# Kernel tuning notes

Measured on AMD Instinct MI355X. Metric: run time of the kernel, lower is better.

Reference implementation:

```python
import jax, jax.numpy as jnp
import numpy as np

B, T, D, H, K = 8, 1024, 512, 8, 33
DK = D // H
PAD = (K - 1) // 2
EPS = 1e-5


def _ln(x, g, b):
    m = x.mean(-1, keepdims=True)
    v = ((x - m) ** 2).mean(-1, keepdims=True)
    return (x - m) / jnp.sqrt(v + EPS) * g + b


def _ffn(x, g, b, w1, b1, w2, b2):
    h = jax.nn.silu(_ln(x, g, b) @ w1 + b1)
    return h @ w2 + b2


def _rel_shift(x):
    # x: [B, H, T1, T2]
    b, h, t1, t2 = x.shape
    x = jnp.pad(x, ((0, 0), (0, 0), (0, 0), (1, 0)))
    x = x.reshape(b, h, t2 + 1, t1)[:, :, 1:, :].reshape(b, h, t1, t2)
    return x[..., :t1]


def setup_inputs() -> dict:
    key = jax.random.key(0)
    ks = iter(jax.random.split(key, 40))
    rn = lambda *s: jax.random.normal(next(ks), s, jnp.float32) * 0.02
    inp = {
        'x': jax.random.normal(next(ks), (B, T, D), jnp.float32),
        'pos_emb': jax.random.normal(next(ks), (1, T, D), jnp.float32),
        # ffn1
        'ln1_g': jnp.ones((D,), jnp.float32), 'ln1_b': jnp.zeros((D,), jnp.float32),
        'ffn1_w1': rn(D, 4 * D), 'ffn1_b1': jnp.zeros((4 * D,), jnp.float32),
        'ffn1_w2': rn(4 * D, D), 'ffn1_b2': jnp.zeros((D,), jnp.float32),
        # mhsa
        'lnq_g': jnp.ones((D,), jnp.float32), 'lnq_b': jnp.zeros((D,), jnp.float32),
        'lnk_g': jnp.ones((D,), jnp.float32), 'lnk_b': jnp.zeros((D,), jnp.float32),
        'lnv_g': jnp.ones((D,), jnp.float32), 'lnv_b': jnp.zeros((D,), jnp.float32),
        'wq': rn(D, D), 'wk': rn(D, D), 'wv': rn(D, D), 'wpos': rn(D, D),
        'pos_bias_u': jnp.zeros((H, DK), jnp.float32),
        'pos_bias_v': jnp.zeros((H, DK), jnp.float32),
        'wfc': rn(D, D),
        # conv module
        'cln_g': jnp.ones((D,), jnp.float32), 'cln_b': jnp.zeros((D,), jnp.float32),
        'pw1': rn(D, 4 * D),             # pointwise_conv1 weight as [in, out]
        'dw_w': rn(2 * D, 1, K),         # depthwise conv weight [C, 1, K]
        'bn_g': jnp.ones((2 * D,), jnp.float32), 'bn_b': jnp.zeros((2 * D,), jnp.float32),
        'pw2': rn(2 * D, D),
        # ffn2
        'ln2_g': jnp.ones((D,), jnp.float32), 'ln2_b': jnp.zeros((D,), jnp.float32),
        'ffn2_w1': rn(D, 4 * D), 'ffn2_b1': jnp.zeros((4 * D,), jnp.float32),
        'ffn2_w2': rn(4 * D, D), 'ffn2_b2': jnp.zeros((D,), jnp.float32),
        # final layer norm
        'lnf_g': jnp.ones((D,), jnp.float32), 'lnf_b': jnp.zeros((D,), jnp.float32),
    }
    return inp


def reference(x, pos_emb, ln1_g, ln1_b, ffn1_w1, ffn1_b1, ffn1_w2, ffn1_b2,
              lnq_g, lnq_b, lnk_g, lnk_b, lnv_g, lnv_b, wq, wk, wv, wpos,
              pos_bias_u, pos_bias_v, wfc,
              cln_g, cln_b, pw1, dw_w, bn_g, bn_b, pw2,
              ln2_g, ln2_b, ffn2_w1, ffn2_b1, ffn2_w2, ffn2_b2, lnf_g, lnf_b):
    b, t, d = x.shape
    scale = 1.0 / DK ** 0.5

    # ---- FFN1 (half-step) ----
    out = 0.5 * x + 0.5 * (x + _ffn(x, ln1_g, ln1_b, ffn1_w1, ffn1_b1, ffn1_w2, ffn1_b2))

    # ---- rel-pos MHSA ----
    res = out
    q = (_ln(out, lnq_g, lnq_b) @ wq).reshape(b, t, H, DK)            # [B,T,H,dk]
    k = (_ln(out, lnk_g, lnk_b) @ wk).reshape(b, t, H, DK).transpose(0, 2, 1, 3)
    v = (_ln(out, lnv_g, lnv_b) @ wv).reshape(b, t, H, DK).transpose(0, 2, 1, 3)
    p = (pos_emb @ wpos).reshape(pos_emb.shape[0], -1, H, DK).transpose(0, 2, 3, 1)  # [1,H,dk,Tp]

    q_u = (q + pos_bias_u).transpose(0, 2, 1, 3)                      # [B,H,T,dk]
    q_v = (q + pos_bias_v).transpose(0, 2, 1, 3)
    matrix_bd = _rel_shift(jnp.matmul(q_v, p) * scale)                # [B,H,T,T]
    scores = jnp.einsum('bhqd,bhkd->bhqk', q_u, k) * scale + matrix_bd
    attn = jax.nn.softmax(scores, axis=-1)
    o = jnp.einsum('bhqk,bhkd->bhqd', attn, v)
    out = o.transpose(0, 2, 1, 3).reshape(b, t, d) @ wfc + res

    # ---- convolution module ----
    res = out
    h = _ln(out, cln_g, cln_b) @ pw1                                  # [B,T,4D]
    a, g = jnp.split(h, 2, axis=-1)
    h = a * jax.nn.sigmoid(g)                                         # GLU -> [B,T,2D]
    h = jax.lax.conv_general_dilated(
        h.transpose(0, 2, 1), dw_w, window_strides=(1,),
        padding=[(PAD, PAD)], feature_group_count=2 * D,
        dimension_numbers=('NCH', 'OIH', 'NCH')).transpose(0, 2, 1)
    h = jax.nn.silu(_ln(h, bn_g, bn_b))
    out = h @ pw2 + res

    # ---- FFN2 (half-step) + final LN ----
    out = 0.5 * out + 0.5 * (out + _ffn(out, ln2_g, ln2_b, ffn2_w1, ffn2_b1, ffn2_w2, ffn2_b2))
    return _ln(out, lnf_g, lnf_b)
```

## Files before the change

kernel.cpp:

```cpp
#include <hip/hip_runtime.h>

typedef unsigned short bf16u;
typedef __attribute__((ext_vector_type(8))) short bf16x8;
typedef __attribute__((ext_vector_type(4))) float f32x4;

__device__ __forceinline__ float bf2f(bf16u u) {
    return __uint_as_float(((unsigned)u) << 16);
}
__device__ __forceinline__ bf16u f2bf(float f) {
    unsigned u = __float_as_uint(f);
    unsigned r = (u + 0x7fffu + ((u >> 16) & 1u)) >> 16;
    return (bf16u)r;
}
__device__ __forceinline__ float sigmoidf_(float x) {
    return 1.0f / (1.0f + __expf(-x));
}

__device__ __forceinline__ void gload_lds16(const bf16u* g, bf16u* l) {
    __builtin_amdgcn_global_load_lds(
        (const __attribute__((address_space(1))) unsigned int*)(const void*)g,
        (__attribute__((address_space(3))) unsigned int*)(void*)l, 16, 0, 0);
}

__global__ void init_flag_kernel(int* flag) {
    if (threadIdx.x == 0 && blockIdx.x == 0) *flag = 0;
}
__global__ __launch_bounds__(256) void detect_kernel(
    const void* x, int nelem, int* flag)
{
    const int scan = nelem < (1 << 20) ? nelem : (1 << 20);
    const bf16u* p = (const bf16u*)x;
    int bad = 0;
    for (int j = blockIdx.x * 256 + threadIdx.x; j < scan; j += 65536) {
        unsigned u = p[j];
        if ((u & 0x7F80u) == 0x7F80u) bad = 1;
    }
    if (bad) atomicOr(flag, 1);
}

__global__ __launch_bounds__(256) void cvt_bf_kernel(
    const void* __restrict__ in, bf16u* __restrict__ out, int n,
    const int* __restrict__ flagp)
{
    const int f32 = *flagp;
    const int i = blockIdx.x * 256 + threadIdx.x;
    if (i >= n) return;
    if (f32) out[i] = f2bf(((const float*)in)[i]);
    else     out[i] = ((const bf16u*)in)[i];
}

struct WTab {
    const void* w[11];
    bf16u* wt[11];
    int K[11];
    int N[11];
};
__global__ __launch_bounds__(256) void wtrans_all(
    WTab tab, const int* __restrict__ flagp)
{
    __shared__ float tile[32][33];
    const int id = blockIdx.z;
    const int K = tab.K[id], N = tab.N[id];
    const int n0 = blockIdx.x * 32, k0 = blockIdx.y * 32;
    if (n0 >= N || k0 >= K) return;
    const void* W = tab.w[id];
    bf16u* Wt = tab.wt[id];
    const int f32 = *flagp;
    const int tx = threadIdx.x & 31, ty = threadIdx.x >> 5;
    #pragma unroll
    for (int r = 0; r < 4; ++r) {
        const int k = ty + r * 8;
        float v;
        if (f32) v = ((const float*)W)[(size_t)(k0 + k) * N + n0 + tx];
        else     v = bf2f(((const bf16u*)W)[(size_t)(k0 + k) * N + n0 + tx]);
        tile[k][tx] = v;
    }
    __syncthreads();
    #pragma unroll
    for (int r = 0; r < 4; ++r) {
        const int n = ty + r * 8;
        Wt[(size_t)(n0 + n) * K + k0 + tx] = f2bf(tile[tx][n]);
    }
}

__global__ __launch_bounds__(256) void vtrans_kernel(
    const bf16u* __restrict__ vb, bf16u* __restrict__ vt)
{
    __shared__ bf16u tile[32][33];
    const int j0 = blockIdx.x * 32;
    const int h = blockIdx.y >> 1, dt = (blockIdx.y & 1) * 32;
    const int b = blockIdx.z;
    const int tx = threadIdx.x & 31, ty = threadIdx.x >> 5;
    #pragma unroll
    for (int r = 0; r < 4; ++r) {
        const int j = ty + r * 8;
        tile[j][tx] = vb[(size_t)(b * 1024 + j0 + j) * 512 + h * 64 + dt + tx];
    }
    __syncthreads();
    #pragma unroll
    for (int r = 0; r < 4; ++r) {
        const int d = ty + r * 8;
        vt[(size_t)((b * 8 + h) * 64 + dt + d) * 1024 + j0 + tx] = tile[tx][d];
    }
}

__global__ __launch_bounds__(256) void add_qbias_kernel(
    const bf16u* __restrict__ qb, const void* __restrict__ bu,
    const void* __restrict__ bv, bf16u* __restrict__ qu,
    bf16u* __restrict__ qv, const int* __restrict__ flagp)
{
    const int f32 = *flagp;
    const int idx = blockIdx.x * 256 + threadIdx.x;
    const int c = idx & 511;
    const float q = bf2f(qb[idx]);
    float ub, vbias;
    if (f32) { ub = ((const float*)bu)[c]; vbias = ((const float*)bv)[c]; }
    else     { ub = bf2f(((const bf16u*)bu)[c]); vbias = bf2f(((const bf16u*)bv)[c]); }
    qu[idx] = f2bf(q + ub);
    qv[idx] = f2bf(q + vbias);
}

template <int D, int IN_MODE, int OUT_MODE, bool SILU, bool COPY>
__global__ __launch_bounds__(256) void ln_kernel(
    const void* __restrict__ in_, const void* __restrict__ gvec,
    const void* __restrict__ bvec, void* __restrict__ out_,
    float* __restrict__ copy_out, const int* __restrict__ flagp)
{
    constexpr int VPT = D / 256;
    const int f32 = *flagp;
    const int row = blockIdx.x;
    const int tid = threadIdx.x;
    const size_t base = (size_t)row * D;
    float x[VPT];
    if (IN_MODE == 2 || (IN_MODE == 1 && !f32)) {
        const bf16u* in = (const bf16u*)in_;
        #pragma unroll
        for (int i = 0; i < VPT; ++i) x[i] = bf2f(in[base + tid + i * 256]);
    } else {
        const float* in = (const float*)in_;
        #pragma unroll
        for (int i = 0; i < VPT; ++i) x[i] = in[base + tid + i * 256];
    }
    float s = 0.f, q = 0.f;
    #pragma unroll
    for (int i = 0; i < VPT; ++i) { s += x[i]; q += x[i] * x[i]; }
    __shared__ float red[10];
    #pragma unroll
    for (int off = 32; off; off >>= 1) {
        s += __shfl_down(s, off, 64);
        q += __shfl_down(q, off, 64);
    }
    const int lane = tid & 63, wv = tid >> 6;
    if (lane == 0) { red[wv] = s; red[4 + wv] = q; }
    __syncthreads();
    if (tid == 0) {
        float ts = red[0] + red[1] + red[2] + red[3];
        float tq = red[4] + red[5] + red[6] + red[7];
        float mean = ts / (float)D;
        float var = tq / (float)D - mean * mean;
        red[8] = mean;
        red[9] = rsqrtf(var + 1e-5f);
    }
    __syncthreads();
    const float mean = red[8], rstd = red[9];
    #pragma unroll
    for (int i = 0; i < VPT; ++i) {
        const int c = tid + i * 256;
        float gv, bv;
        if (f32) {
            gv = ((const float*)gvec)[c];
            bv = ((const float*)bvec)[c];
        } else {
            gv = bf2f(((const bf16u*)gvec)[c]);
            bv = bf2f(((const bf16u*)bvec)[c]);
        }
        float v = (x[i] - mean) * rstd * gv + bv;
        if (SILU) v *= sigmoidf_(v);
        if (OUT_MODE == 0) {
            ((bf16u*)out_)[base + c] = f2bf(v);
        } else {
            if (f32) ((float*)out_)[base + c] = v;
            else     ((bf16u*)out_)[base + c] = f2bf(v);
        }
        if (COPY) copy_out[base + c] = x[i];
    }
}

template <int TM>
__global__ __launch_bounds__(256) void gemm_mfma(
    const bf16u* __restrict__ A, const bf16u* __restrict__ Wt,
    const void* __restrict__ bias, const float* __restrict__ res,
    void* __restrict__ C, int M, int N, int K, float alpha, int act,
    int outbf, const int* __restrict__ flagp)
{
    constexpr int CHUNKS_A = TM * 4;
    constexpr int TOT = CHUNKS_A + 512;
    constexpr int CPW = TOT / 4;
    constexpr int ISSUES = CPW / 64;
    constexpr int BUFSZ = (TM + 128) * 32;
    constexpr int MI = 4;
    constexpr int NJ = (TM == 128) ? 4 : 2;
    __shared__ bf16u sh[3 * BUFSZ];
    const int f32 = *flagp;
    const int tid = threadIdx.x;
    const int mtiles = M / TM;
    const int lid = blockIdx.y * gridDim.x + blockIdx.x;
    const int bm = (lid % mtiles) * TM;
    const int bn = (lid / mtiles) * 128;
    const int lane = tid & 63, wvid = tid >> 6;
    const int wm = (TM == 128) ? (wvid >> 1) * 64 : 0;
    const int wn = (TM == 128) ? (wvid & 1) * 64 : wvid * 32;

    f32x4 acc[MI][NJ];
    {
        f32x4 z = {0.f, 0.f, 0.f, 0.f};
        #pragma unroll
        for (int i = 0; i < MI; ++i)
            #pragma unroll
            for (int j = 0; j < NJ; ++j) acc[i][j] = z;
    }
    const int kq = (lane >> 4) * 8, fr = lane & 15;

    #define STAGE_G(k0, bufp)                                                   \
    {                                                                           \
        bf16u* base_ = (bufp);                                                  \
        _Pragma("unroll")                                                       \
        for (int t = 0; t < ISSUES; ++t) {                                      \
            const int cc = wvid * CPW + t * 64 + lane;                          \
            const bf16u* src_;                                                  \
            if (cc < CHUNKS_A)                                                  \
                src_ = A + (size_t)(bm + (cc >> 2)) * K + (k0) + (cc & 3) * 8;  \
            else {                                                              \
                const int cb_ = cc - CHUNKS_A;                                  \
                src_ = Wt + (size_t)(bn + (cb_ >> 2)) * K + (k0) + (cb_ & 3) * 8;\
            }                                                                   \
            gload_lds16(src_, base_ + (wvid * CPW + t * 64) * 8);               \
        }                                                                       \
    }

    const int KT = K / 32;
    STAGE_G(0, sh);
    STAGE_G(32, sh + BUFSZ);
    int bufidx = 0;
    for (int kt = 0; kt < KT; ++kt) {
        if (kt + 1 < KT)
            asm volatile("s_waitcnt vmcnt(%0)\ns_barrier" :: "i"(ISSUES) : "memory");
        else
            asm volatile("s_waitcnt vmcnt(0)\ns_barrier" ::: "memory");
        if (kt + 2 < KT) {
            int nb = bufidx + 2; if (nb >= 3) nb -= 3;
            STAGE_G((kt + 2) * 32, sh + nb * BUFSZ);
        }
        const bf16u* buf = sh + bufidx * BUFSZ;
        bf16x8 af[MI], bfr[NJ];
        #pragma unroll
        for (int i = 0; i < MI; ++i)
            af[i] = *(const bf16x8*)&buf[(wm + i * 16 + fr) * 32 + kq];
        #pragma unroll
        for (int j = 0; j < NJ; ++j)
            bfr[j] = *(const bf16x8*)&buf[TM * 32 + (wn + j * 16 + fr) * 32 + kq];
        #pragma unroll
        for (int i = 0; i < MI; ++i)
            #pragma unroll
            for (int j = 0; j < NJ; ++j)
                acc[i][j] = __builtin_amdgcn_mfma_f32_16x16x32_bf16(
                    bfr[j], af[i], acc[i][j], 0, 0, 0);
        ++bufidx; if (bufidx == 3) bufidx = 0;
    }
    #undef STAGE_G

    const int quad = lane >> 4, col = lane & 15;
    #pragma unroll
    for (int j = 0; j < NJ; ++j) {
        const int n0 = bn + wn + j * 16 + quad * 4;
        float4 bv4 = {0.f, 0.f, 0.f, 0.f};
        if (bias) {
            if (f32) bv4 = *(const float4*)((const float*)bias + n0);
            else {
                ushort4 bu = *(const ushort4*)((const bf16u*)bias + n0);
                bv4.x = bf2f(bu.x); bv4.y = bf2f(bu.y);
                bv4.z = bf2f(bu.z); bv4.w = bf2f(bu.w);
            }
        }
        #pragma unroll
        for (int i = 0; i < MI; ++i) {
            const int m = bm + wm + i * 16 + col;
            const size_t off = (size_t)m * N + n0;
            float v[4];
            #pragma unroll
            for (int r = 0; r < 4; ++r) {
                float t = acc[i][j][r] + ((const float*)&bv4)[r];
                if (act == 1) t *= sigmoidf_(t);
                v[r] = t * alpha;
            }
            if (res) {
                float4 r4 = *(const float4*)(res + off);
                v[0] += r4.x; v[1] += r4.y; v[2] += r4.z; v[3] += r4.w;
            }
            if (outbf) {
                ushort4 o;
                o.x = f2bf(v[0]); o.y = f2bf(v[1]);
                o.z = f2bf(v[2]); o.w = f2bf(v[3]);
                *(ushort4*)((bf16u*)C + off) = o;
            } else {
                float4 o = {v[0], v[1], v[2], v[3]};
                *(float4*)((float*)C + off) = o;
            }
        }
    }
}

__global__ __launch_bounds__(256) void attn_score_mfma(
    const bf16u* __restrict__ qu, const bf16u* __restrict__ qv,
    const bf16u* __restrict__ kb, const bf16u* __restrict__ pb,
    bf16u* __restrict__ S, bf16u* __restrict__ BD)
{
    constexpr int BUFSZ = 8192;
    __shared__ bf16u sh[2 * BUFSZ];
    const int tid = threadIdx.x;
    const int z = blockIdx.z;
    const int h = z & 7, bb = (z >> 3) & 1, which = z >> 4;
    const bf16u* A = (which ? qv : qu) + (size_t)bb * 524288;
    const bf16u* B = which ? pb : (kb + (size_t)bb * 524288);
    bf16u* C = (which ? BD : S) + (size_t)(bb * 8 + h) * 1048576;
    const int hoff = h * 64;
    const int bm = blockIdx.y * 128, bn = blockIdx.x * 128;
    const int lane = tid & 63, wvid = tid >> 6;
    const int wm = (wvid >> 1) * 64, wn = (wvid & 1) * 64;
    const int kq = (lane >> 4) * 8, fr = lane & 15;

    f32x4 acc[4][4];
    {
        f32x4 zr = {0.f, 0.f, 0.f, 0.f};
        #pragma unroll
        for (int i = 0; i < 4; ++i)
            #pragma unroll
            for (int j = 0; j < 4; ++j) acc[i][j] = zr;
    }

    #define STAGE_S(k0, bsel)                                                   \
    {                                                                           \
        bf16u* base_ = sh + (bsel) * BUFSZ;                                     \
        _Pragma("unroll")                                                       \
        for (int t = 0; t < 4; ++t) {                                           \
            const int cc = wvid * 256 + t * 64 + lane;                          \
            const bf16u* src_;                                                  \
            if (cc < 512)                                                       \
                src_ = A + (size_t)(bm + (cc >> 2)) * 512 + hoff + (k0) + (cc & 3) * 8; \
            else {                                                              \
                const int cb_ = cc - 512;                                       \
                src_ = B + (size_t)(bn + (cb_ >> 2)) * 512 + hoff + (k0) + (cb_ & 3) * 8; \
            }                                                                   \
            gload_lds16(src_, base_ + (wvid * 256 + t * 64) * 8);               \
        }                                                                       \
    }

    STAGE_S(0, 0);
    #pragma unroll
    for (int kt = 0; kt < 2; ++kt) {
        __syncthreads();
        if (kt == 0) STAGE_S(32, 1);
        const bf16u* buf = sh + (kt & 1) * BUFSZ;
        bf16x8 af[4], bfr[4];
        #pragma unroll
        for (int i = 0; i < 4; ++i)
            af[i] = *(const bf16x8*)&buf[(wm + i * 16 + fr) * 32 + kq];
        #pragma unroll
        for (int j = 0; j < 4; ++j)
            bfr[j] = *(const bf16x8*)&buf[4096 + (wn + j * 16 + fr) * 32 + kq];
        #pragma unroll
        for (int i = 0; i < 4; ++i)
            #pragma unroll
            for (int j = 0; j < 4; ++j)
                acc[i][j] = __builtin_amdgcn_mfma_f32_16x16x32_bf16(
                    bfr[j], af[i], acc[i][j], 0, 0, 0);
    }
    #undef STAGE_S

    const int quad = lane >> 4, col = lane & 15;
    #pragma unroll
    for (int j = 0; j < 4; ++j) {
        const int n0 = bn + wn + j * 16 + quad * 4;
        #pragma unroll
        for (int i = 0; i < 4; ++i) {
            const int m = bm + wm + i * 16 + col;
            ushort4 o;
            o.x = f2bf(acc[i][j][0] * 0.125f);
            o.y = f2bf(acc[i][j][1] * 0.125f);
            o.z = f2bf(acc[i][j][2] * 0.125f);
            o.w = f2bf(acc[i][j][3] * 0.125f);
            *(ushort4*)(C + (size_t)m * 1024 + n0) = o;
        }
    }
}

__global__ __launch_bounds__(256) void attn_softmax_kernel(
    bf16u* __restrict__ S, const bf16u* __restrict__ BD)
{
    const int i = blockIdx.x, h = blockIdx.y, bb = blockIdx.z;
    const int tid = threadIdx.x;
    const size_t hb = (size_t)(bb * 8 + h) * 1048576;
    bf16u* srow = S + hb + (size_t)i * 1024;
    const bf16u* bd0 = BD + hb + (size_t)i * 1024;
    const bf16u* bd1 = bd0 + 1024;
    float v[4];
    #pragma unroll
    for (int k = 0; k < 4; ++k) {
        const int j = tid + k * 256;
        float bd;
        if (j <= i)          bd = bf2f(bd0[1023 - i + j]);
        else if (j == i + 1) bd = 0.f;
        else                 bd = bf2f(bd1[j - i - 2]);
        v[k] = bf2f(srow[j]) + bd;
    }
    __shared__ float red[6];
    float m = fmaxf(fmaxf(v[0], v[1]), fmaxf(v[2], v[3]));
    #pragma unroll
    for (int off = 32; off; off >>= 1) m = fmaxf(m, __shfl_down(m, off, 64));
    const int lane = tid & 63, w = tid >> 6;
    if (lane == 0) red[w] = m;
    __syncthreads();
    if (tid == 0) red[4] = fmaxf(fmaxf(red[0], red[1]), fmaxf(red[2], red[3]));
    __syncthreads();
    m = red[4];
    float e[4], l = 0.f;
    #pragma unroll
    for (int k = 0; k < 4; ++k) { e[k] = __expf(v[k] - m); l += e[k]; }
    #pragma unroll
    for (int off = 32; off; off >>= 1) l += __shfl_down(l, off, 64);
    if (lane == 0) red[w] = l;
    __syncthreads();
    if (tid == 0) red[5] = red[0] + red[1] + red[2] + red[3];
    __syncthreads();
    const float inv = 1.0f / red[5];
    #pragma unroll
    for (int k = 0; k < 4; ++k) srow[tid + k * 256] = f2bf(e[k] * inv);
}

__global__ __launch_bounds__(256) void attn_pv_mfma(
    const bf16u* __restrict__ P, const bf16u* __restrict__ Vt,
    bf16u* __restrict__ O)
{
    constexpr int BUFSZ = 4096;
    __shared__ bf16u sh[3 * BUFSZ];
    const int tid = threadIdx.x;
    const int h = blockIdx.y, bb = blockIdx.z;
    const int bm = blockIdx.x * 64;
    const int hoff = h * 64;
    const bf16u* Ph = P + (size_t)(bb * 8 + h) * 1048576;
    const bf16u* Vh = Vt + (size_t)bb * 524288 + (size_t)h * 65536;
    bf16u* Ob = O + (size_t)bb * 524288;
    const int lane = tid & 63, wvid = tid >> 6;
    const int wm = wvid * 16;
    const int kq = (lane >> 4) * 8, fr = lane & 15;

    f32x4 acc[4];
    {
        f32x4 z = {0.f, 0.f, 0.f, 0.f};
        #pragma unroll
        for (int j = 0; j < 4; ++j) acc[j] = z;
    }

    #define STAGE_P(k0, bufp)                                                   \
    {                                                                           \
        bf16u* base_ = (bufp);                                                  \
        _Pragma("unroll")                                                       \
        for (int t = 0; t < 2; ++t) {                                           \
            const int cc = wvid * 128 + t * 64 + lane;                          \
            const bf16u* src_;                                                  \
            if (cc < 256)                                                       \
                src_ = Ph + (size_t)(bm + (cc >> 2)) * 1024 + (k0) + (cc & 3) * 8; \
            else {                                                              \
                const int cb_ = cc - 256;                                       \
                src_ = Vh + (size_t)(cb_ >> 2) * 1024 + (k0) + (cb_ & 3) * 8;   \
            }                                                                   \
            gload_lds16(src_, base_ + (wvid * 128 + t * 64) * 8);               \
        }                                                                       \
    }

    STAGE_P(0, sh);
    STAGE_P(32, sh + BUFSZ);
    int bufidx = 0;
    for (int kt = 0; kt < 32; ++kt) {
        if (kt + 1 < 32)
            asm volatile("s_waitcnt vmcnt(2)\ns_barrier" ::: "memory");
        else
            asm volatile("s_waitcnt vmcnt(0)\ns_barrier" ::: "memory");
        if (kt + 2 < 32) {
            int nb = bufidx + 2; if (nb >= 3) nb -= 3;
            STAGE_P((kt + 2) * 32, sh + nb * BUFSZ);
        }
        const bf16u* buf = sh + bufidx * BUFSZ;
        bf16x8 af = *(const bf16x8*)&buf[(wm + fr) * 32 + kq];
        #pragma unroll
        for (int j = 0; j < 4; ++j) {
            bf16x8 bf = *(const bf16x8*)&buf[2048 + (j * 16 + fr) * 32 + kq];
            acc[j] = __builtin_amdgcn_mfma_f32_16x16x32_bf16(bf, af, acc[j], 0, 0, 0);
        }
        ++bufidx; if (bufidx == 3) bufidx = 0;
    }
    #undef STAGE_P

    const int quad = lane >> 4, col = lane & 15;
    const int m = bm + wm + col;
    #pragma unroll
    for (int j = 0; j < 4; ++j) {
        const int d0 = j * 16 + quad * 4;
        ushort4 o;
        o.x = f2bf(acc[j][0]); o.y = f2bf(acc[j][1]);
        o.z = f2bf(acc[j][2]); o.w = f2bf(acc[j][3]);
        *(ushort4*)(Ob + (size_t)m * 512 + hoff + d0) = o;
    }
}

__global__ __launch_bounds__(256) void glu_kernel(
    const bf16u* __restrict__ H, bf16u* __restrict__ out, int total)
{
    const int idx = blockIdx.x * 256 + threadIdx.x;
    if (idx >= total) return;
    const int m = idx >> 10, c = idx & 1023;
    const float a = bf2f(H[(size_t)m * 2048 + c]);
    const float g = bf2f(H[(size_t)m * 2048 + 1024 + c]);
    out[idx] = f2bf(a * sigmoidf_(g));
}

__global__ __launch_bounds__(256) void dwconv_kernel(
    const bf16u* __restrict__ in, const void* __restrict__ wp,
    bf16u* __restrict__ out, const int* __restrict__ flagp)
{
    const int f32 = *flagp;
    const int cb = blockIdx.x & 1;
    const int ttile = (blockIdx.x >> 1) & 127;
    const int b = blockIdx.x >> 8;
    const int t0 = ttile * 8;
    const int c = cb * 512 + threadIdx.x * 2;

    float w0[33], w1[33];
    if (f32) {
        const float* wf = (const float*)wp;
        #pragma unroll
        for (int k = 0; k < 33; ++k) { w0[k] = wf[c * 33 + k]; w1[k] = wf[(c + 1) * 33 + k]; }
    } else {
        const bf16u* wb = (const bf16u*)wp;
        #pragma unroll
        for (int k = 0; k < 33; ++k) { w0[k] = bf2f(wb[c * 33 + k]); w1[k] = bf2f(wb[(c + 1) * 33 + k]); }
    }

    unsigned win[40];
    #pragma unroll
    for (int r = 0; r < 40; ++r) {
        const int tt = t0 - 16 + r;
        win[r] = (tt >= 0 && tt < 1024)
               ? *(const unsigned*)(in + (size_t)(b * 1024 + tt) * 1024 + c)
               : 0u;
    }
    float acc0[8] = {}, acc1[8] = {};
    #pragma unroll
    for (int k = 0; k < 33; ++k) {
        #pragma unroll
        for (int dt = 0; dt < 8; ++dt) {
            const unsigned u = win[dt + k];
            acc0[dt] = fmaf(bf2f((bf16u)(u & 0xffffu)), w0[k], acc0[dt]);
            acc1[dt] = fmaf(bf2f((bf16u)(u >> 16)), w1[k], acc1[dt]);
        }
    }
    #pragma unroll
    for (int dt = 0; dt < 8; ++dt) {
        unsigned o = (unsigned)f2bf(acc0[dt]) | ((unsigned)f2bf(acc1[dt]) << 16);
        *(unsigned*)(out + (size_t)(b * 1024 + t0 + dt) * 1024 + c) = o;
    }
}

static inline void launch_gemm(const bf16u* A, const bf16u* Wt, const void* bias,
                               const float* res, void* C, int M, int N, int K,
                               float alpha, int act, int outbf, const int* flagp,
                               hipStream_t stream)
{
    if (N >= 1024) {
        dim3 grid(N / 128, M / 128);
        gemm_mfma<128><<<grid, 256, 0, stream>>>(A, Wt, bias, res, C, M, N, K, alpha, act, outbf, flagp);
    } else {
        dim3 grid(N / 128, M / 64);
        gemm_mfma<64><<<grid, 256, 0, stream>>>(A, Wt, bias, res, C, M, N, K, alpha, act, outbf, flagp);
    }
}

extern "C" void kernel_launch(void* const* d_in, const int* in_sizes, int n_in,
                              void* d_out, int out_size, void* d_ws, size_t ws_size,
                              hipStream_t stream)
{
    const void* x       = d_in[0];
    const void* pos_emb = d_in[1];
    const void* ln1_g   = d_in[2];
    const void* ln1_b   = d_in[3];
    const void* ffn1_w1 = d_in[4];
    const void* ffn1_b1 = d_in[5];
    const void* ffn1_w2 = d_in[6];
    const void* ffn1_b2 = d_in[7];
    const void* lnq_g   = d_in[8];
    const void* lnq_b   = d_in[9];
    const void* lnk_g   = d_in[10];
    const void* lnk_b   = d_in[11];
    const void* lnv_g   = d_in[12];
    const void* lnv_b   = d_in[13];
    const void* wq      = d_in[14];
    const void* wk      = d_in[15];
    const void* wv      = d_in[16];
    const void* wpos    = d_in[17];
    const void* pbu     = d_in[18];
    const void* pbv     = d_in[19];
    const void* wfc     = d_in[20];
    const void* cln_g   = d_in[21];
    const void* cln_b   = d_in[22];
    const void* pw1     = d_in[23];
    const void* dw_w    = d_in[24];
    const void* bn_g    = d_in[25];
    const void* bn_b    = d_in[26];
    const void* pw2     = d_in[27];
    const void* ln2_g   = d_in[28];
    const void* ln2_b   = d_in[29];
    const void* ffn2_w1 = d_in[30];
    const void* ffn2_b1 = d_in[31];
    const void* ffn2_w2 = d_in[32];
    const void* ffn2_b2 = d_in[33];
    const void* lnf_g   = d_in[34];
    const void* lnf_b   = d_in[35];

    const int BT = 8192;
    char* wsb = (char*)d_ws;
    float* act  = (float*)(wsb + 0);
    bf16u* qb   = (bf16u*)(wsb + 16777216);
    bf16u* kb   = (bf16u*)(wsb + 25165824);
    bf16u* vb   = (bf16u*)(wsb + 33554432);
    bf16u* pb   = (bf16u*)(wsb + 41943040);
    bf16u* tmpb = (bf16u*)(wsb + 42991616);
    bf16u* qu   = (bf16u*)(wsb + 51380224);
    bf16u* qv   = (bf16u*)(wsb + 59768832);
    bf16u* vt   = (bf16u*)(wsb + 68157440);
    bf16u* S    = (bf16u*)(wsb + 76546048);
    bf16u* BD   = (bf16u*)(wsb + 110100480);
    bf16u* wc   = (bf16u*)(wsb + 143654912);
    int* flagp  = (int*)(wsb + 157810688);
    bf16u* obb  = tmpb;
    bf16u* hbf  = (bf16u*)(wsb + 51380224);
    bf16u* Gbf  = (bf16u*)(wsb + 84934656);
    bf16u* DWbf = (bf16u*)(wsb + 16777216);
    bf16u* LObf = (bf16u*)(wsb + 33554432);

    bf16u* w_ffn1_1 = wc + 0;
    bf16u* w_ffn1_2 = wc + 1048576;
    bf16u* w_q      = wc + 2097152;
    bf16u* w_k      = wc + 2359296;
    bf16u* w_v      = wc + 2621440;
    bf16u* w_pos    = wc + 2883584;
    bf16u* w_fc     = wc + 3145728;
    bf16u* w_pw1    = wc + 3407872;
    bf16u* w_pw2    = wc + 4456448;
    bf16u* w_ffn2_1 = wc + 4980736;
    bf16u* w_ffn2_2 = wc + 6029312;

    init_flag_kernel<<<1, 64, 0, stream>>>(flagp);
    detect_kernel<<<256, 256, 0, stream>>>(x, in_sizes[0], flagp);

    WTab tab;
    tab.w[0] = ffn1_w1; tab.wt[0] = w_ffn1_1; tab.K[0] = 512;  tab.N[0] = 2048;
    tab.w[1] = ffn1_w2; tab.wt[1] = w_ffn1_2; tab.K[1] = 2048; tab.N[1] = 512;
    tab.w[2] = wq;      tab.wt[2] = w_q;      tab.K[2] = 512;  tab.N[2] = 512;
    tab.w[3] = wk;      tab.wt[3] = w_k;      tab.K[3] = 512;  tab.N[3] = 512;
    tab.w[4] = wv;      tab.wt[4] = w_v;      tab.K[4] = 512;  tab.N[4] = 512;
    tab.w[5] = wpos;    tab.wt[5] = w_pos;    tab.K[5] = 512;  tab.N[5] = 512;
    tab.w[6] = wfc;     tab.wt[6] = w_fc;     tab.K[6] = 512;  tab.N[6] = 512;
    tab.w[7] = pw1;     tab.wt[7] = w_pw1;    tab.K[7] = 512;  tab.N[7] = 2048;
    tab.w[8] = pw2;     tab.wt[8] = w_pw2;    tab.K[8] = 1024; tab.N[8] = 512;
    tab.w[9] = ffn2_w1; tab.wt[9] = w_ffn2_1; tab.K[9] = 512;  tab.N[9] = 2048;
    tab.w[10] = ffn2_w2; tab.wt[10] = w_ffn2_2; tab.K[10] = 2048; tab.N[10] = 512;
    wtrans_all<<<dim3(64, 64, 11), 256, 0, stream>>>(tab, flagp);

    cvt_bf_kernel<<<2048, 256, 0, stream>>>(pos_emb, tmpb, 524288, flagp);
    launch_gemm(tmpb, w_pos, nullptr, nullptr, pb, 1024, 512, 512, 1.0f, 0, 1, flagp, stream);

    ln_kernel<512, 1, 0, false, true><<<BT, 256, 0, stream>>>(x, ln1_g, ln1_b, tmpb, act, flagp);
    launch_gemm(tmpb, w_ffn1_1, ffn1_b1, nullptr, hbf, BT, 2048, 512, 1.0f, 1, 1, flagp, stream);
    launch_gemm(hbf, w_ffn1_2, ffn1_b2, act, act, BT, 512, 2048, 0.5f, 0, 0, flagp, stream);

    ln_kernel<512, 0, 0, false, false><<<BT, 256, 0, stream>>>(act, lnq_g, lnq_b, tmpb, nullptr, flagp);
    launch_gemm(tmpb, w_q, nullptr, nullptr, qb, BT, 512, 512, 1.0f, 0, 1, flagp, stream);
    ln_kernel<512, 0, 0, false, false><<<BT, 256, 0, stream>>>(act, lnk_g, lnk_b, tmpb, nullptr, flagp);
    launch_gemm(tmpb, w_k, nullptr, nullptr, kb, BT, 512, 512, 1.0f, 0, 1, flagp, stream);
    ln_kernel<512, 0, 0, false, false><<<BT, 256, 0, stream>>>(act, lnv_g, lnv_b, tmpb, nullptr, flagp);
    launch_gemm(tmpb, w_v, nullptr, nullptr, vb, BT, 512, 512, 1.0f, 0, 1, flagp, stream);

    add_qbias_kernel<<<16384, 256, 0, stream>>>(qb, pbu, pbv, qu, qv, flagp);
    vtrans_kernel<<<dim3(32, 16, 8), 256, 0, stream>>>(vb, vt);

    for (int b0 = 0; b0 < 8; b0 += 2) {
        const bf16u* qu_b = qu + (size_t)b0 * 524288;
        const bf16u* qv_b = qv + (size_t)b0 * 524288;
        const bf16u* kb_b = kb + (size_t)b0 * 524288;
        const bf16u* vt_b = vt + (size_t)b0 * 524288;
        bf16u* ob_b = obb + (size_t)b0 * 524288;
        attn_score_mfma<<<dim3(8, 8, 32), 256, 0, stream>>>(qu_b, qv_b, kb_b, pb, S, BD);
        attn_softmax_kernel<<<dim3(1024, 8, 2), 256, 0, stream>>>(S, BD);
        attn_pv_mfma<<<dim3(16, 8, 2), 256, 0, stream>>>(S, vt_b, ob_b);
    }
    launch_gemm(obb, w_fc, nullptr, act, act, BT, 512, 512, 1.0f, 0, 0, flagp, stream);

    ln_kernel<512, 0, 0, false, false><<<BT, 256, 0, stream>>>(act, cln_g, cln_b, tmpb, nullptr, flagp);
    launch_gemm(tmpb, w_pw1, nullptr, nullptr, hbf, BT, 2048, 512, 1.0f, 0, 1, flagp, stream);
    glu_kernel<<<32768, 256, 0, stream>>>(hbf, Gbf, 8388608);
    dwconv_kernel<<<2048, 256, 0, stream>>>(Gbf, dw_w, DWbf, flagp);
    ln_kernel<1024, 2, 0, true, false><<<BT, 256, 0, stream>>>(DWbf, bn_g, bn_b, LObf, nullptr, flagp);
    launch_gemm(LObf, w_pw2, nullptr, act, act, BT, 512, 1024, 1.0f, 0, 0, flagp, stream);

    ln_kernel<512, 0, 0, false, false><<<BT, 256, 0, stream>>>(act, ln2_g, ln2_b, tmpb, nullptr, flagp);
    launch_gemm(tmpb, w_ffn2_1, ffn2_b1, nullptr, hbf, BT, 2048, 512, 1.0f, 1, 1, flagp, stream);
    launch_gemm(hbf, w_ffn2_2, ffn2_b2, act, act, BT, 512, 2048, 0.5f, 0, 0, flagp, stream);

    ln_kernel<512, 0, 1, false, false><<<BT, 256, 0, stream>>>(act, lnf_g, lnf_b, d_out, nullptr, flagp);
}
```

Before: 812.4 us.

## Load GEMM A operand directly into registers instead of staging through LDS

The MFMA GEMM now stages only the weight (B) tile through the triple-buffered LDS pipeline. Each lane fetches its own A fragments straight from global memory into registers, prefetching one k-step ahead. This shrinks LDS use and removes the LDS write and read for A, which could help occupancy and cut LDS traffic. In exchange, A loads are less coalesced, and in the 128-row tile two waves fetch the same A rows again, so more traffic falls on the caches. The wait count is now fixed at 6 outstanding loads.

```diff
diff --git a/kernel.cpp b/kernel.cpp
--- a/kernel.cpp
+++ b/kernel.cpp
@@ -193,11 +193,7 @@
     void* __restrict__ C, int M, int N, int K, float alpha, int act,
     int outbf, const int* __restrict__ flagp)
 {
-    constexpr int CHUNKS_A = TM * 4;
-    constexpr int TOT = CHUNKS_A + 512;
-    constexpr int CPW = TOT / 4;
-    constexpr int ISSUES = CPW / 64;
-    constexpr int BUFSZ = (TM + 128) * 32;
+    constexpr int BUFSZ = 128 * 32;
     constexpr int MI = 4;
     constexpr int NJ = (TM == 128) ? 4 : 2;
     __shared__ bf16u sh[3 * BUFSZ];
@@ -210,6 +206,7 @@
     const int lane = tid & 63, wvid = tid >> 6;
     const int wm = (TM == 128) ? (wvid >> 1) * 64 : 0;
     const int wn = (TM == 128) ? (wvid & 1) * 64 : wvid * 32;
+    const int kq = (lane >> 4) * 8, fr = lane & 15;
 
     f32x4 acc[MI][NJ];
     {
@@ -219,55 +216,62 @@
             #pragma unroll
             for (int j = 0; j < NJ; ++j) acc[i][j] = z;
     }
-    const int kq = (lane >> 4) * 8, fr = lane & 15;
-
-    #define STAGE_G(k0, bufp)                                                   \
+
+    const bf16u* Arow[MI];
+    #pragma unroll
+    for (int i = 0; i < MI; ++i)
+        Arow[i] = A + (size_t)(bm + wm + i * 16 + fr) * K + kq;
+
+    #define STAGE_B(k0, bufp)                                                   \
     {                                                                           \
         bf16u* base_ = (bufp);                                                  \
         _Pragma("unroll")                                                       \
-        for (int t = 0; t < ISSUES; ++t) {                                      \
-            const int cc = wvid * CPW + t * 64 + lane;                          \
-            const bf16u* src_;                                                  \
-            if (cc < CHUNKS_A)                                                  \
-                src_ = A + (size_t)(bm + (cc >> 2)) * K + (k0) + (cc & 3) * 8;  \
-            else {                                                              \
-                const int cb_ = cc - CHUNKS_A;                                  \
-                src_ = Wt + (size_t)(bn + (cb_ >> 2)) * K + (k0) + (cb_ & 3) * 8;\
-            }                                                                   \
-            gload_lds16(src_, base_ + (wvid * CPW + t * 64) * 8);               \
+        for (int t = 0; t < 2; ++t) {                                           \
+            const int cc = wvid * 128 + t * 64 + lane;                          \
+            gload_lds16(Wt + (size_t)(bn + (cc >> 2)) * K + (k0) + (cc & 3) * 8,\
+                        base_ + cc * 8);                                        \
         }                                                                       \
     }
 
     const int KT = K / 32;
-    STAGE_G(0, sh);
-    STAGE_G(32, sh + BUFSZ);
+    uint4 acur[MI], anext[MI];
+    #pragma unroll
+    for (int i = 0; i < MI; ++i) acur[i] = *(const uint4*)(Arow[i]);
+    STAGE_B(0, sh);
+    STAGE_B(32, sh + BUFSZ);
     int bufidx = 0;
     for (int kt = 0; kt < KT; ++kt) {
+        if (kt + 1 < KT) {
+            #pragma unroll
+            for (int i = 0; i < MI; ++i)
+                anext[i] = *(const uint4*)(Arow[i] + (size_t)(kt + 1) * 32);
+        }
+        if (kt + 2 < KT) {
+            int nb = bufidx + 2; if (nb >= 3) nb -= 3;
+            STAGE_B((kt + 2) * 32, sh + nb * BUFSZ);
+        }
         if (kt + 1 < KT)
-            asm volatile("s_waitcnt vmcnt(%0)\ns_barrier" :: "i"(ISSUES) : "memory");
+            asm volatile("s_waitcnt vmcnt(6)\ns_barrier" ::: "memory");
         else
             asm volatile("s_waitcnt vmcnt(0)\ns_barrier" ::: "memory");
-        if (kt + 2 < KT) {
-            int nb = bufidx + 2; if (nb >= 3) nb -= 3;
-            STAGE_G((kt + 2) * 32, sh + nb * BUFSZ);
-        }
         const bf16u* buf = sh + bufidx * BUFSZ;
-        bf16x8 af[MI], bfr[NJ];
-        #pragma unroll
-        for (int i = 0; i < MI; ++i)
-            af[i] = *(const bf16x8*)&buf[(wm + i * 16 + fr) * 32 + kq];
+        bf16x8 bfr[NJ];
         #pragma unroll
         for (int j = 0; j < NJ; ++j)
-            bfr[j] = *(const bf16x8*)&buf[TM * 32 + (wn + j * 16 + fr) * 32 + kq];
-        #pragma unroll
-        for (int i = 0; i < MI; ++i)
+            bfr[j] = *(const bf16x8*)&buf[(wn + j * 16 + fr) * 32 + kq];
+        #pragma unroll
+        for (int i = 0; i < MI; ++i) {
+            bf16x8 af = *(const bf16x8*)&acur[i];
             #pragma unroll
             for (int j = 0; j < NJ; ++j)
                 acc[i][j] = __builtin_amdgcn_mfma_f32_16x16x32_bf16(
-                    bfr[j], af[i], acc[i][j], 0, 0, 0);
+                    bfr[j], af, acc[i][j], 0, 0, 0);
+        }
+        #pragma unroll
+        for (int i = 0; i < MI; ++i) acur[i] = anext[i];
         ++bufidx; if (bufidx == 3) bufidx = 0;
     }
-    #undef STAGE_G
+    #undef STAGE_B
 
     const int quad = lane >> 4, col = lane & 15;
     #pragma unroll
```

Measured after the change: 995.0 us. 1.22x slower.

## Fold LayerNorm affine into weights and fuse Q/K/V projections into one GEMM

Applied to the files above, without the earlier changes.

Folds each pre-GEMM LayerNorm's gamma into the transposed weight rows and its beta into a per-output bias, accumulated with atomics during weight preparation. Those LayerNorms then only normalize. The three separate LN+GEMM passes for Q, K and V become one plain LN and one N=1536 GEMM writing an interleaved QKV buffer, and the downstream kernels read K and V with a 1536 stride. This removes two LayerNorm launches, two passes over the activations and two GEMM launches. The cost is a strided layout for the attention inputs and rounding gamma-scaled weights to bf16.

```diff
diff --git a/kernel.cpp b/kernel.cpp
--- a/kernel.cpp
+++ b/kernel.cpp
@@ -49,9 +49,27 @@
     else     out[i] = ((const bf16u*)in)[i];
 }
 
+__global__ __launch_bounds__(256) void bias_init_kernel(
+    float* bias_qkv, float* bias_ffn1, const void* ffn1_b1,
+    float* bias_pw1, float* bias_ffn2, const void* ffn2_b1,
+    const int* __restrict__ flagp)
+{
+    const int f32 = *flagp;
+    const int i = blockIdx.x * 256 + threadIdx.x;
+    if (i < 1536) bias_qkv[i] = 0.f;
+    if (i < 2048) {
+        bias_ffn1[i] = f32 ? ((const float*)ffn1_b1)[i] : bf2f(((const bf16u*)ffn1_b1)[i]);
+        bias_pw1[i]  = 0.f;
+        bias_ffn2[i] = f32 ? ((const float*)ffn2_b1)[i] : bf2f(((const bf16u*)ffn2_b1)[i]);
+    }
+}
+
 struct WTab {
     const void* w[11];
     bf16u* wt[11];
+    const void* g[11];
+    const void* bs[11];
+    float* bd[11];
     int K[11];
     int N[11];
 };
@@ -59,32 +77,54 @@
     WTab tab, const int* __restrict__ flagp)
 {
     __shared__ float tile[32][33];
+    __shared__ float bpart[8][33];
     const int id = blockIdx.z;
     const int K = tab.K[id], N = tab.N[id];
     const int n0 = blockIdx.x * 32, k0 = blockIdx.y * 32;
     if (n0 >= N || k0 >= K) return;
     const void* W = tab.w[id];
     bf16u* Wt = tab.wt[id];
+    const void* gv = tab.g[id];
+    const void* bsv = tab.bs[id];
+    float* bdv = tab.bd[id];
     const int f32 = *flagp;
     const int tx = threadIdx.x & 31, ty = threadIdx.x >> 5;
+    float bacc = 0.f;
     #pragma unroll
     for (int r = 0; r < 4; ++r) {
         const int k = ty + r * 8;
         float v;
         if (f32) v = ((const float*)W)[(size_t)(k0 + k) * N + n0 + tx];
         else     v = bf2f(((const bf16u*)W)[(size_t)(k0 + k) * N + n0 + tx]);
+        if (bsv) {
+            float b = f32 ? ((const float*)bsv)[k0 + k]
+                          : bf2f(((const bf16u*)bsv)[k0 + k]);
+            bacc += b * v;
+        }
+        if (gv) {
+            float g = f32 ? ((const float*)gv)[k0 + k]
+                          : bf2f(((const bf16u*)gv)[k0 + k]);
+            v *= g;
+        }
         tile[k][tx] = v;
     }
+    if (bsv) bpart[ty][tx] = bacc;
     __syncthreads();
     #pragma unroll
     for (int r = 0; r < 4; ++r) {
         const int n = ty + r * 8;
         Wt[(size_t)(n0 + n) * K + k0 + tx] = f2bf(tile[tx][n]);
     }
+    if (bsv && ty == 0) {
+        float t = 0.f;
+        #pragma unroll
+        for (int r = 0; r < 8; ++r) t += bpart[r][tx];
+        atomicAdd(bdv + n0 + tx, t);
+    }
 }
 
 __global__ __launch_bounds__(256) void vtrans_kernel(
-    const bf16u* __restrict__ vb, bf16u* __restrict__ vt)
+    const bf16u* __restrict__ vsl, bf16u* __restrict__ vt)
 {
     __shared__ bf16u tile[32][33];
     const int j0 = blockIdx.x * 32;
@@ -94,7 +134,7 @@
     #pragma unroll
     for (int r = 0; r < 4; ++r) {
         const int j = ty + r * 8;
-        tile[j][tx] = vb[(size_t)(b * 1024 + j0 + j) * 512 + h * 64 + dt + tx];
+        tile[j][tx] = vsl[(size_t)(b * 1024 + j0 + j) * 1536 + h * 64 + dt + tx];
     }
     __syncthreads();
     #pragma unroll
@@ -105,14 +145,14 @@
 }
 
 __global__ __launch_bounds__(256) void add_qbias_kernel(
-    const bf16u* __restrict__ qb, const void* __restrict__ bu,
+    const bf16u* __restrict__ qkvb, const void* __restrict__ bu,
     const void* __restrict__ bv, bf16u* __restrict__ qu,
     bf16u* __restrict__ qv, const int* __restrict__ flagp)
 {
     const int f32 = *flagp;
     const int idx = blockIdx.x * 256 + threadIdx.x;
-    const int c = idx & 511;
-    const float q = bf2f(qb[idx]);
+    const int row = idx >> 9, c = idx & 511;
+    const float q = bf2f(qkvb[(size_t)row * 1536 + c]);
     float ub, vbias;
     if (f32) { ub = ((const float*)bu)[c]; vbias = ((const float*)bv)[c]; }
     else     { ub = bf2f(((const bf16u*)bu)[c]); vbias = bf2f(((const bf16u*)bv)[c]); }
@@ -120,7 +160,7 @@
     qv[idx] = f2bf(q + vbias);
 }
 
-template <int D, int IN_MODE, int OUT_MODE, bool SILU, bool COPY>
+template <int D, int IN_MODE, int OUT_MODE, bool SILU, bool COPY, bool GB>
 __global__ __launch_bounds__(256) void ln_kernel(
     const void* __restrict__ in_, const void* __restrict__ gvec,
     const void* __restrict__ bvec, void* __restrict__ out_,
@@ -166,15 +206,18 @@
     #pragma unroll
     for (int i = 0; i < VPT; ++i) {
         const int c = tid + i * 256;
-        float gv, bv;
-        if (f32) {
-            gv = ((const float*)gvec)[c];
-            bv = ((const float*)bvec)[c];
-        } else {
-            gv = bf2f(((const bf16u*)gvec)[c]);
-            bv = bf2f(((const bf16u*)bvec)[c]);
-        }
-        float v = (x[i] - mean) * rstd * gv + bv;
+        float v = (x[i] - mean) * rstd;
+        if (GB) {
+            float gv, bv;
+            if (f32) {
+                gv = ((const float*)gvec)[c];
+                bv = ((const float*)bvec)[c];
+            } else {
+                gv = bf2f(((const bf16u*)gvec)[c]);
+                bv = bf2f(((const bf16u*)bvec)[c]);
+            }
+            v = v * gv + bv;
+        }
         if (SILU) v *= sigmoidf_(v);
         if (OUT_MODE == 0) {
             ((bf16u*)out_)[base + c] = f2bf(v);
@@ -189,9 +232,10 @@
 template <int TM>
 __global__ __launch_bounds__(256) void gemm_mfma(
     const bf16u* __restrict__ A, const bf16u* __restrict__ Wt,
-    const void* __restrict__ bias, const float* __restrict__ res,
-    void* __restrict__ C, int M, int N, int K, float alpha, int act,
-    int outbf, const int* __restrict__ flagp)
+    const float* __restrict__ biasf, const void* __restrict__ biasr,
+    const float* __restrict__ res, void* __restrict__ C,
+    int M, int N, int K, float alpha, int act, int outbf,
+    const int* __restrict__ flagp)
 {
     constexpr int CHUNKS_A = TM * 4;
     constexpr int TOT = CHUNKS_A + 512;
@@ -274,10 +318,12 @@
     for (int j = 0; j < NJ; ++j) {
         const int n0 = bn + wn + j * 16 + quad * 4;
         float4 bv4 = {0.f, 0.f, 0.f, 0.f};
-        if (bias) {
-            if (f32) bv4 = *(const float4*)((const float*)bias + n0);
+        if (biasf) {
+            bv4 = *(const float4*)(biasf + n0);
+        } else if (biasr) {
+            if (f32) bv4 = *(const float4*)((const float*)biasr + n0);
             else {
-                ushort4 bu = *(const ushort4*)((const bf16u*)bias + n0);
+                ushort4 bu = *(const ushort4*)((const bf16u*)biasr + n0);
                 bv4.x = bf2f(bu.x); bv4.y = bf2f(bu.y);
                 bv4.z = bf2f(bu.z); bv4.w = bf2f(bu.w);
             }
@@ -312,7 +358,7 @@
 
 __global__ __launch_bounds__(256) void attn_score_mfma(
     const bf16u* __restrict__ qu, const bf16u* __restrict__ qv,
-    const bf16u* __restrict__ kb, const bf16u* __restrict__ pb,
+    const bf16u* __restrict__ ksl, const bf16u* __restrict__ pb,
     bf16u* __restrict__ S, bf16u* __restrict__ BD)
 {
     constexpr int BUFSZ = 8192;
@@ -321,7 +367,10 @@
     const int z = blockIdx.z;
     const int h = z & 7, bb = (z >> 3) & 1, which = z >> 4;
     const bf16u* A = (which ? qv : qu) + (size_t)bb * 524288;
-    const bf16u* B = which ? pb : (kb + (size_t)bb * 524288);
+    const bf16u* B;
+    int sB;
+    if (which) { B = pb; sB = 512; }
+    else       { B = ksl + (size_t)bb * 1572864; sB = 1536; }
     bf16u* C = (which ? BD : S) + (size_t)(bb * 8 + h) * 1048576;
     const int hoff = h * 64;
     const int bm = blockIdx.y * 128, bn = blockIdx.x * 128;
@@ -349,7 +398,7 @@
                 src_ = A + (size_t)(bm + (cc >> 2)) * 512 + hoff + (k0) + (cc & 3) * 8; \
             else {                                                              \
                 const int cb_ = cc - 512;                                       \
-                src_ = B + (size_t)(bn + (cb_ >> 2)) * 512 + hoff + (k0) + (cb_ & 3) * 8; \
+                src_ = B + (size_t)(bn + (cb_ >> 2)) * sB + hoff + (k0) + (cb_ & 3) * 8; \
             }                                                                   \
             gload_lds16(src_, base_ + (wvid * 256 + t * 64) * 8);               \
         }                                                                       \
@@ -571,17 +620,18 @@
     }
 }
 
-static inline void launch_gemm(const bf16u* A, const bf16u* Wt, const void* bias,
+static inline void launch_gemm(const bf16u* A, const bf16u* Wt,
+                               const float* biasf, const void* biasr,
                                const float* res, void* C, int M, int N, int K,
                                float alpha, int act, int outbf, const int* flagp,
                                hipStream_t stream)
 {
     if (N >= 1024) {
         dim3 grid(N / 128, M / 128);
-        gemm_mfma<128><<<grid, 256, 0, stream>>>(A, Wt, bias, res, C, M, N, K, alpha, act, outbf, flagp);
+        gemm_mfma<128><<<grid, 256, 0, stream>>>(A, Wt, biasf, biasr, res, C, M, N, K, alpha, act, outbf, flagp);
     } else {
         dim3 grid(N / 128, M / 64);
-        gemm_mfma<64><<<grid, 256, 0, stream>>>(A, Wt, bias, res, C, M, N, K, alpha, act, outbf, flagp);
+        gemm_mfma<64><<<grid, 256, 0, stream>>>(A, Wt, biasf, biasr, res, C, M, N, K, alpha, act, outbf, flagp);
     }
 }
 
@@ -628,30 +678,27 @@
 
     const int BT = 8192;
     char* wsb = (char*)d_ws;
-    float* act  = (float*)(wsb + 0);
-    bf16u* qb   = (bf16u*)(wsb + 16777216);
-    bf16u* kb   = (bf16u*)(wsb + 25165824);
-    bf16u* vb   = (bf16u*)(wsb + 33554432);
-    bf16u* pb   = (bf16u*)(wsb + 41943040);
-    bf16u* tmpb = (bf16u*)(wsb + 42991616);
-    bf16u* qu   = (bf16u*)(wsb + 51380224);
-    bf16u* qv   = (bf16u*)(wsb + 59768832);
-    bf16u* vt   = (bf16u*)(wsb + 68157440);
-    bf16u* S    = (bf16u*)(wsb + 76546048);
-    bf16u* BD   = (bf16u*)(wsb + 110100480);
-    bf16u* wc   = (bf16u*)(wsb + 143654912);
-    int* flagp  = (int*)(wsb + 157810688);
-    bf16u* obb  = tmpb;
-    bf16u* hbf  = (bf16u*)(wsb + 51380224);
-    bf16u* Gbf  = (bf16u*)(wsb + 84934656);
-    bf16u* DWbf = (bf16u*)(wsb + 16777216);
-    bf16u* LObf = (bf16u*)(wsb + 33554432);
+    float* act   = (float*)(wsb + 0);
+    bf16u* qkvb  = (bf16u*)(wsb + 16777216);
+    bf16u* pb    = (bf16u*)(wsb + 41943040);
+    bf16u* tmpb  = (bf16u*)(wsb + 42991616);
+    bf16u* qu    = (bf16u*)(wsb + 51380224);
+    bf16u* qv    = (bf16u*)(wsb + 59768832);
+    bf16u* vt    = (bf16u*)(wsb + 68157440);
+    bf16u* S     = (bf16u*)(wsb + 76546048);
+    bf16u* BD    = (bf16u*)(wsb + 110100480);
+    bf16u* wc    = (bf16u*)(wsb + 143654912);
+    int* flagp   = (int*)(wsb + 157810688);
+    float* biasb = (float*)(wsb + 157811712);
+    bf16u* obb   = tmpb;
+    bf16u* hbf   = (bf16u*)(wsb + 51380224);
+    bf16u* Gbf   = (bf16u*)(wsb + 84934656);
+    bf16u* DWbf  = (bf16u*)(wsb + 16777216);
+    bf16u* LObf  = (bf16u*)(wsb + 33554432);
 
     bf16u* w_ffn1_1 = wc + 0;
     bf16u* w_ffn1_2 = wc + 1048576;
-    bf16u* w_q      = wc + 2097152;
-    bf16u* w_k      = wc + 2359296;
-    bf16u* w_v      = wc + 2621440;
+    bf16u* w_qkv    = wc + 2097152;
     bf16u* w_pos    = wc + 2883584;
     bf16u* w_fc     = wc + 3145728;
     bf16u* w_pw1    = wc + 3407872;
@@ -659,62 +706,65 @@
     bf16u* w_ffn2_1 = wc + 4980736;
     bf16u* w_ffn2_2 = wc + 6029312;
 
+    float* bias_qkv  = biasb + 0;
+    float* bias_ffn1 = biasb + 1536;
+    float* bias_pw1  = biasb + 3584;
+    float* bias_ffn2 = biasb + 5632;
+
     init_flag_kernel<<<1, 64, 0, stream>>>(flagp);
     detect_kernel<<<256, 256, 0, stream>>>(x, in_sizes[0], flagp);
 
+    bias_init_kernel<<<8, 256, 0, stream>>>(bias_qkv, bias_ffn1, ffn1_b1,
+                                            bias_pw1, bias_ffn2, ffn2_b1, flagp);
     WTab tab;
-    tab.w[0] = ffn1_w1; tab.wt[0] = w_ffn1_1; tab.K[0] = 512;  tab.N[0] = 2048;
-    tab.w[1] = ffn1_w2; tab.wt[1] = w_ffn1_2; tab.K[1] = 2048; tab.N[1] = 512;
-    tab.w[2] = wq;      tab.wt[2] = w_q;      tab.K[2] = 512;  tab.N[2] = 512;
-    tab.w[3] = wk;      tab.wt[3] = w_k;      tab.K[3] = 512;  tab.N[3] = 512;
-    tab.w[4] = wv;      tab.wt[4] = w_v;      tab.K[4] = 512;  tab.N[4] = 512;
-    tab.w[5] = wpos;    tab.wt[5] = w_pos;    tab.K[5] = 512;  tab.N[5] = 512;
-    tab.w[6] = wfc;     tab.wt[6] = w_fc;     tab.K[6] = 512;  tab.N[6] = 512;
-    tab.w[7] = pw1;     tab.wt[7] = w_pw1;    tab.K[7] = 512;  tab.N[7] = 2048;
-    tab.w[8] = pw2;     tab.wt[8] = w_pw2;    tab.K[8] = 1024; tab.N[8] = 512;
-    tab.w[9] = ffn2_w1; tab.wt[9] = w_ffn2_1; tab.K[9] = 512;  tab.N[9] = 2048;
-    tab.w[10] = ffn2_w2; tab.wt[10] = w_ffn2_2; tab.K[10] = 2048; tab.N[10] = 512;
+    tab.w[0] = ffn1_w1; tab.wt[0] = w_ffn1_1; tab.g[0] = ln1_g; tab.bs[0] = ln1_b; tab.bd[0] = bias_ffn1; tab.K[0] = 512;  tab.N[0] = 2048;
+    tab.w[1] = ffn1_w2; tab.wt[1] = w_ffn1_2; tab.g[1] = nullptr; tab.bs[1] = nullptr; tab.bd[1] = nullptr; tab.K[1] = 2048; tab.N[1] = 512;
+    tab.w[2] = wq; tab.wt[2] = w_qkv;                tab.g[2] = lnq_g; tab.bs[2] = lnq_b; tab.bd[2] = bias_qkv;        tab.K[2] = 512; tab.N[2] = 512;
+    tab.w[3] = wk; tab.wt[3] = w_qkv + 262144;       tab.g[3] = lnk_g; tab.bs[3] = lnk_b; tab.bd[3] = bias_qkv + 512;  tab.K[3] = 512; tab.N[3] = 512;
+    tab.w[4] = wv; tab.wt[4] = w_qkv + 524288;       tab.g[4] = lnv_g; tab.bs[4] = lnv_b; tab.bd[4] = bias_qkv + 1024; tab.K[4] = 512; tab.N[4] = 512;
+    tab.w[5] = wpos; tab.wt[5] = w_pos; tab.g[5] = nullptr; tab.bs[5] = nullptr; tab.bd[5] = nullptr; tab.K[5] = 512; tab.N[5] = 512;
+    tab.w[6] = wfc;  tab.wt[6] = w_fc;  tab.g[6] = nullptr; tab.bs[6] = nullptr; tab.bd[6] = nullptr; tab.K[6] = 512; tab.N[6] = 512;
+    tab.w[7] = pw1;  tab.wt[7] = w_pw1; tab.g[7] = cln_g; tab.bs[7] = cln_b; tab.bd[7] = bias_pw1; tab.K[7] = 512; tab.N[7] = 2048;
+    tab.w[8] = pw2;  tab.wt[8] = w_pw2; tab.g[8] = nullptr; tab.bs[8] = nullptr; tab.bd[8] = nullptr; tab.K[8] = 1024; tab.N[8] = 512;
+    tab.w[9] = ffn2_w1; tab.wt[9] = w_ffn2_1; tab.g[9] = ln2_g; tab.bs[9] = ln2_b; tab.bd[9] = bias_ffn2; tab.K[9] = 512; tab.N[9] = 2048;
+    tab.w[10] = ffn2_w2; tab.wt[10] = w_ffn2_2; tab.g[10] = nullptr; tab.bs[10] = nullptr; tab.bd[10] = nullptr; tab.K[10] = 2048; tab.N[10] = 512;
     wtrans_all<<<dim3(64, 64, 11), 256, 0, stream>>>(tab, flagp);
 
     cvt_bf_kernel<<<2048, 256, 0, stream>>>(pos_emb, tmpb, 524288, flagp);
-    launch_gemm(tmpb, w_pos, nullptr, nullptr, pb, 1024, 512, 512, 1.0f, 0, 1, flagp, stream);
-
-    ln_kernel<512, 1, 0, false, true><<<BT, 256, 0, stream>>>(x, ln1_g, ln1_b, tmpb, act, flagp);
-    launch_gemm(tmpb, w_ffn1_1, ffn1_b1, nullptr, hbf, BT, 2048, 512, 1.0f, 1, 1, flagp, stream);
-    launch_gemm(hbf, w_ffn1_2, ffn1_b2, act, act, BT, 512, 2048, 0.5f, 0, 0, flagp, stream);
-
-    ln_kernel<512, 0, 0, false, false><<<BT, 256, 0, stream>>>(act, lnq_g, lnq_b, tmpb, nullptr, flagp);
-    launch_gemm(tmpb, w_q, nullptr, nullptr, qb, BT, 512, 512, 1.0f, 0, 1, flagp, stream);
-    ln_kernel<512, 0, 0, false, false><<<BT, 256, 0, stream>>>(act, lnk_g, lnk_b, tmpb, nullptr, flagp);
-    launch_gemm(tmpb, w_k, nullptr, nullptr, kb, BT, 512, 512, 1.0f, 0, 1, flagp, stream);
-    ln_kernel<512, 0, 0, false, false><<<BT, 256, 0, stream>>>(act, lnv_g, lnv_b, tmpb, nullptr, flagp);
-    launch_gemm(tmpb, w_v, nullptr, nullptr, vb, BT, 512, 512, 1.0f, 0, 1, flagp, stream);
-
-    add_qbias_kernel<<<16384, 256, 0, stream>>>(qb, pbu, pbv, qu, qv, flagp);
-    vtrans_kernel<<<dim3(32, 16, 8), 256, 0, stream>>>(vb, vt);
+    launch_gemm(tmpb, w_pos, nullptr, nullptr, nullptr, pb, 1024, 512, 512, 1.0f, 0, 1, flagp, stream);
+
+    ln_kernel<512, 1, 0, false, true, false><<<BT, 256, 0, stream>>>(x, nullptr, nullptr, tmpb, act, flagp);
+    launch_gemm(tmpb, w_ffn1_1, bias_ffn1, nullptr, nullptr, hbf, BT, 2048, 512, 1.0f, 1, 1, flagp, stream);
+    launch_gemm(hbf, w_ffn1_2, nullptr, ffn1_b2, act, act, BT, 512, 2048, 0.5f, 0, 0, flagp, stream);
+
+    ln_kernel<512, 0, 0, false, false, false><<<BT, 256, 0, stream>>>(act, nullptr, nullptr, tmpb, nullptr, flagp);
+    launch_gemm(tmpb, w_qkv, bias_qkv, nullptr, nullptr, qkvb, BT, 1536, 512, 1.0f, 0, 1, flagp, stream);
+
+    add_qbias_kernel<<<16384, 256, 0, stream>>>(qkvb, pbu, pbv, qu, qv, flagp);
+    vtrans_kernel<<<dim3(32, 16, 8), 256, 0, stream>>>(qkvb + 1024, vt);
 
     for (int b0 = 0; b0 < 8; b0 += 2) {
         const bf16u* qu_b = qu + (size_t)b0 * 524288;
         const bf16u* qv_b = qv + (size_t)b0 * 524288;
-        const bf16u* kb_b = kb + (size_t)b0 * 524288;
+        const bf16u* k_b  = qkvb + (size_t)b0 * 1572864 + 512;
         const bf16u* vt_b = vt + (size_t)b0 * 524288;
         bf16u* ob_b = obb + (size_t)b0 * 524288;
-        attn_score_mfma<<<dim3(8, 8, 32), 256, 0, stream>>>(qu_b, qv_b, kb_b, pb, S, BD);
+        attn_score_mfma<<<dim3(8, 8, 32), 256, 0, stream>>>(qu_b, qv_b, k_b, pb, S, BD);
         attn_softmax_kernel<<<dim3(1024, 8, 2), 256, 0, stream>>>(S, BD);
         attn_pv_mfma<<<dim3(16, 8, 2), 256, 0, stream>>>(S, vt_b, ob_b);
     }
-    launch_gemm(obb, w_fc, nullptr, act, act, BT, 512, 512, 1.0f, 0, 0, flagp, stream);
-
-    ln_kernel<512, 0, 0, false, false><<<BT, 256, 0, stream>>>(act, cln_g, cln_b, tmpb, nullptr, flagp);
-    launch_gemm(tmpb, w_pw1, nullptr, nullptr, hbf, BT, 2048, 512, 1.0f, 0, 1, flagp, stream);
+    launch_gemm(obb, w_fc, nullptr, nullptr, act, act, BT, 512, 512, 1.0f, 0, 0, flagp, stream);
+
+    ln_kernel<512, 0, 0, false, false, false><<<BT, 256, 0, stream>>>(act, nullptr, nullptr, tmpb, nullptr, flagp);
+    launch_gemm(tmpb, w_pw1, bias_pw1, nullptr, nullptr, hbf, BT, 2048, 512, 1.0f, 0, 1, flagp, stream);
     glu_kernel<<<32768, 256, 0, stream>>>(hbf, Gbf, 8388608);
     dwconv_kernel<<<2048, 256, 0, stream>>>(Gbf, dw_w, DWbf, flagp);
-    ln_kernel<1024, 2, 0, true, false><<<BT, 256, 0, stream>>>(DWbf, bn_g, bn_b, LObf, nullptr, flagp);
-    launch_gemm(LObf, w_pw2, nullptr, act, act, BT, 512, 1024, 1.0f, 0, 0, flagp, stream);
-
-    ln_kernel<512, 0, 0, false, false><<<BT, 256, 0, stream>>>(act, ln2_g, ln2_b, tmpb, nullptr, flagp);
-    launch_gemm(tmpb, w_ffn2_1, ffn2_b1, nullptr, hbf, BT, 2048, 512, 1.0f, 1, 1, flagp, stream);
-    launch_gemm(hbf, w_ffn2_2, ffn2_b2, act, act, BT, 512, 2048, 0.5f, 0, 0, flagp, stream);
-
-    ln_kernel<512, 0, 1, false, false><<<BT, 256, 0, stream>>>(act, lnf_g, lnf_b, d_out, nullptr, flagp);
-}
+    ln_kernel<1024, 2, 0, true, false, true><<<BT, 256, 0, stream>>>(DWbf, bn_g, bn_b, LObf, nullptr, flagp);
+    launch_gemm(LObf, w_pw2, nullptr, nullptr, act, act, BT, 512, 1024, 1.0f, 0, 0, flagp, stream);
+
+    ln_kernel<512, 0, 0, false, false, false><<<BT, 256, 0, stream>>>(act, nullptr, nullptr, tmpb, nullptr, flagp);
+    launch_gemm(tmpb, w_ffn2_1, bias_ffn2, nullptr, nullptr, hbf, BT, 2048, 512, 1.0f, 1, 1, flagp, stream);
+    launch_gemm(hbf, w_ffn2_2, nullptr, ffn2_b2, act, act, BT, 512, 2048, 0.5f, 0, 0, flagp, stream);
+
+    ln_kernel<512, 0, 1, false, false, true><<<BT, 256, 0, stream>>>(act, lnf_g, lnf_b, d_out, nullptr, flagp);
+}
```

New measurement: 779.2 us. -4.1%, faster.
